# Kernel optimization log

Hardware: AMD Instinct MI355X
Metric: run time of the kernel (lower is better)

## Reference

```python
import jax, jax.numpy as jnp
import numpy as np


def sym_logm(x):
    # matrix log of symmetric positive-definite matrices via eigh
    w, v = jnp.linalg.eigh(x)
    return jnp.einsum('...ik,...k,...jk->...ij', v, jnp.log(w), v)


def olm_diffeo(x):
    s = sym_logm(x)
    L = jnp.tril(s, -1)
    return L + L.swapaxes(-1, -2)


def cayley_map(X):
    I = jnp.eye(X.shape[-1], dtype=X.dtype)
    return (I - X) @ jnp.linalg.inv(I + X)


def trans_base(W, y):
    # C = cayley(skew(W)); y -> sym off-diagonal part of C y C^T
    C = cayley_map(W - W.T)
    y = jnp.einsum('pq,bnqr,sr->bnps', C, y, C)
    L = jnp.tril(y, -1)
    return L + L.swapaxes(-1, -2)


def setup_inputs() -> dict:
    B, N, n = 16, 512, 32
    key = jax.random.key(0)
    k1, k2, k3, k4 = jax.random.split(key, 4)
    A = jax.random.normal(k1, (B, N, n, n), dtype=jnp.float32)
    cov = A @ A.swapaxes(-1, -2) / n + jnp.eye(n, dtype=jnp.float32)
    d = jnp.sqrt(jnp.diagonal(cov, axis1=-2, axis2=-1))
    x = cov / (d[..., :, None] * d[..., None, :])  # SPD correlation matrices
    q_weight = jax.random.normal(k2, (n, n), dtype=jnp.float32) * 2.0 - 1.0
    k_weight = jax.random.normal(k3, (n, n), dtype=jnp.float32) * 2.0 - 1.0
    v_weight = jax.random.normal(k4, (n, n), dtype=jnp.float32) * 2.0 - 1.0
    return {"x": x, "q_weight": q_weight, "k_weight": k_weight, "v_weight": v_weight}


def reference(x, q_weight, k_weight, v_weight):
    xl = olm_diffeo(x)                       # [B,N,n,n]
    q = trans_base(q_weight, xl)
    k = trans_base(k_weight, xl)
    v = trans_base(v_weight, xl)
    B, N, n, _ = q.shape
    qf = q.reshape(B, N, n * n)
    kf = k.reshape(B, N, n * n)
    # energy[b,j,i] = ||q_i - k_j||_F  (Gram trick instead of [B,N,N,n,n] broadcast)
    q2 = jnp.sum(qf * qf, axis=-1)
    k2 = jnp.sum(kf * kf, axis=-1)
    d2 = q2[:, None, :] + k2[:, :, None] - 2.0 * jnp.einsum('bjf,bif->bji', kf, qf)
    energy = jnp.sqrt(jnp.maximum(d2, 1e-12))
    scores = 1.0 / (1.0 + jnp.log1p(energy))
    p = jax.nn.softmax(scores, axis=-2)      # softmax over j (dim -2), as in torch
    attn = p.swapaxes(-1, -2)                # [b, i, j]
    # out[b,c] = sum_a v[b,a] * attn[b,a,c]  (faithful to torch broadcast+sum(dim=1))
    return jnp.einsum('bac,baij->bcij', attn, v)
```

## Files before the change

kernel.cpp:

```cpp
#include <hip/hip_runtime.h>
#include <math.h>

#define NB 16
#define NSQ 512
#define NMAT (NB*NSQ)
#define NF 1024
#define NSWEEP 7
#define SB 36

__global__ __launch_bounds__(64) void cayley_kernel(
    const float* __restrict__ qw, const float* __restrict__ kw,
    const float* __restrict__ vw, float* __restrict__ Cout) {
  __shared__ float M[32][33];
  __shared__ float R[32][33];
  __shared__ float fac[32];
  const float* W = (blockIdx.x == 0) ? qw : ((blockIdx.x == 1) ? kw : vw);
  const int t = threadIdx.x;
  for (int idx = t; idx < 1024; idx += 64) {
    int i = idx >> 5, j = idx & 31;
    float xv = W[i*32+j] - W[j*32+i];
    float d = (i == j) ? 1.0f : 0.0f;
    M[i][j] = d - xv;
    R[i][j] = d + xv;
  }
  __syncthreads();
  for (int k = 0; k < 32; ++k) {
    float inv = 1.0f / M[k][k];
    __syncthreads();
    if (t < 32) M[k][t] *= inv; else R[k][t-32] *= inv;
    __syncthreads();
    if (t < 32) fac[t] = M[t][k];
    __syncthreads();
    if (t < 32) {
      float mk = M[k][t];
      for (int i = 0; i < 32; ++i) {
        if (i == k) continue;
        M[i][t] -= fac[i] * mk;
      }
    } else {
      int tc = t - 32;
      float rk = R[k][tc];
      for (int i = 0; i < 32; ++i) {
        if (i == k) continue;
        R[i][tc] -= fac[i] * rk;
      }
    }
    __syncthreads();
  }
  for (int idx = t; idx < 1024; idx += 64) {
    int p = idx >> 5, q = idx & 31;
    Cout[blockIdx.x * 1024 + idx] = R[q][p];
  }
}

__global__ __launch_bounds__(128) void logm_qkv_kernel(
    const float* __restrict__ x, const float* __restrict__ Cm,
    float* __restrict__ qo, float* __restrict__ ko, float* __restrict__ vo,
    float* __restrict__ q2, float* __restrict__ k2) {
  __shared__ __align__(16) float buf0[32*SB];
  __shared__ __align__(16) float buf1[32*SB];
  __shared__ __align__(16) float buf2[32*SB];
  __shared__ __align__(16) float2 cs[16];
  __shared__ __align__(16) float lw[32];
  __shared__ float wsum[2];
  const int t = threadIdx.x;
  const int m = blockIdx.x;
  const float* xm = x + (size_t)m * NF;

  #pragma unroll
  for (int s = 0; s < 2; ++s) {
    int fi = t + 128*s;
    int i = fi >> 3, j4 = (fi & 7) << 2;
    float4 xv = *(const float4*)&xm[(size_t)fi*4];
    *(float4*)&buf0[i*SB + j4] = xv;
    float4 iv;
    iv.x = (i == j4+0) ? 1.0f : 0.0f;
    iv.y = (i == j4+1) ? 1.0f : 0.0f;
    iv.z = (i == j4+2) ? 1.0f : 0.0f;
    iv.w = (i == j4+3) ? 1.0f : 0.0f;
    *(float4*)&buf1[i*SB + j4] = iv;
  }
  __syncthreads();

  const int abase = t >> 4;
  const int bI = t & 15;
  const int pi = abase & 1;

  for (int sw = 0; sw < NSWEEP; ++sw) {
    for (int r = 1; r < 32; ++r) {
      const int h = 31 - __builtin_clz((unsigned)r);
      const int lowmask = (1 << h) - 1;
      if (t < 16) {
        int p = ((t >> h) << (h+1)) | (t & lowmask);
        int q = p ^ r;
        float apq = buf0[p*SB+q];
        float c = 1.0f, s = 0.0f;
        if (fabsf(apq) > 1e-36f) {
          float app = buf0[p*SB+p];
          float aqq = buf0[q*SB+q];
          float tau = (aqq - app) / (2.0f * apq);
          float tt = 1.0f / (fabsf(tau) + sqrtf(1.0f + tau*tau));
          tt = (tau < 0.0f) ? -tt : tt;
          c = 1.0f / sqrtf(1.0f + tt*tt);
          s = tt * c;
        }
        cs[t] = make_float2(c, s);
      }
      __syncthreads();
      if (r == 1) {
        {
          int pr = t >> 3;
          int ch = (t & 7) << 2;
          int p = pr << 1;
          int q = p | 1;
          float2 c2 = cs[pr];
          float4 ap = *(float4*)&buf0[p*SB + ch];
          float4 aq = *(float4*)&buf0[q*SB + ch];
          float4 np, nq;
          np.x = c2.x*ap.x - c2.y*aq.x;  nq.x = fmaf(c2.y, ap.x, c2.x*aq.x);
          np.y = c2.x*ap.y - c2.y*aq.y;  nq.y = fmaf(c2.y, ap.y, c2.x*aq.y);
          np.z = c2.x*ap.z - c2.y*aq.z;  nq.z = fmaf(c2.y, ap.z, c2.x*aq.z);
          np.w = c2.x*ap.w - c2.y*aq.w;  nq.w = fmaf(c2.y, ap.w, c2.x*aq.w);
          *(float4*)&buf0[p*SB + ch] = np;
          *(float4*)&buf0[q*SB + ch] = nq;
        }
        __syncthreads();
        #pragma unroll
        for (int s4 = 0; s4 < 2; ++s4) {
          int tsk = t + 128*s4;
          int i = tsk >> 3;
          int cch = tsk & 7;
          float2 cA = cs[2*cch];
          float2 cB = cs[2*cch+1];
          float4 y = *(float4*)&buf0[i*SB + 4*cch];
          float4 z;
          z.x = cA.x*y.x - cA.y*y.y;  z.y = fmaf(cA.y, y.x, cA.x*y.y);
          z.z = cB.x*y.z - cB.y*y.w;  z.w = fmaf(cB.y, y.z, cB.x*y.w);
          *(float4*)&buf0[i*SB + 4*cch] = z;
        }
      } else {
        int pb = ((bI >> h) << (h+1)) | (bI & lowmask);
        int qb = pb ^ r;
        if (pi) { int tmp = pb; pb = qb; qb = tmp; }
        const float2 cb2 = cs[bI];
        const float cbb = cb2.x;
        const float sbb = pi ? -cb2.y : cb2.y;
        #pragma unroll
        for (int u = 0; u < 2; ++u) {
          int a = abase + 8*u;
          int pa = ((a >> h) << (h+1)) | (a & lowmask);
          int qa = pa ^ r;
          if (pi) { int tmp = pa; pa = qa; qa = tmp; }
          float2 ca2 = cs[a];
          float caa = ca2.x;
          float saa = pi ? -ca2.y : ca2.y;
          float* rp = buf0 + pa*SB;
          float* rq = buf0 + qa*SB;
          float x11 = rp[pb], x12 = rp[qb];
          float x21 = rq[pb], x22 = rq[qb];
          float y11 = caa*x11 - saa*x21;
          float y12 = caa*x12 - saa*x22;
          float y21 = fmaf(saa, x11, caa*x21);
          float y22 = fmaf(saa, x12, caa*x22);
          rp[pb] = cbb*y11 - sbb*y12;
          rp[qb] = fmaf(sbb, y11, cbb*y12);
          rq[pb] = cbb*y21 - sbb*y22;
          rq[qb] = fmaf(sbb, y21, cbb*y22);
        }
      }
      {
        int pr = t >> 3;
        int ch = (t & 7) << 2;
        int p = ((pr >> h) << (h+1)) | (pr & lowmask);
        int q = p ^ r;
        float2 c2 = cs[pr];
        float4 vp = *(float4*)&buf1[p*SB + ch];
        float4 vq = *(float4*)&buf1[q*SB + ch];
        float4 np, nq;
        np.x = c2.x*vp.x - c2.y*vq.x;  nq.x = fmaf(c2.y, vp.x, c2.x*vq.x);
        np.y = c2.x*vp.y - c2.y*vq.y;  nq.y = fmaf(c2.y, vp.y, c2.x*vq.y);
        np.z = c2.x*vp.z - c2.y*vq.z;  nq.z = fmaf(c2.y, vp.z, c2.x*vq.z);
        np.w = c2.x*vp.w - c2.y*vq.w;  nq.w = fmaf(c2.y, vp.w, c2.x*vq.w);
        *(float4*)&buf1[p*SB + ch] = np;
        *(float4*)&buf1[q*SB + ch] = nq;
      }
      __syncthreads();
    }
  }

  if (t < 32) lw[t] = logf(fmaxf(buf0[t*SB+t], 1e-30f));
  __syncthreads();
  #pragma unroll
  for (int s = 0; s < 8; ++s) {
    int idx = t + 128*s;
    int i = idx >> 5, k = idx & 31;
    buf0[i*SB + k] = buf1[k*SB + i];
  }
  __syncthreads();

  const int rg = t >> 4, cg = t & 15;
  const int i0 = rg*4, j0 = cg*2;
  {
    float acc[4][2] = {};
    #pragma unroll
    for (int k4 = 0; k4 < 32; k4 += 4) {
      float4 lv = *(float4*)&lw[k4];
      float4 av[4], bv[2];
      #pragma unroll
      for (int d = 0; d < 4; ++d) {
        float4 a4 = *(float4*)&buf0[(i0+d)*SB + k4];
        av[d].x = a4.x*lv.x; av[d].y = a4.y*lv.y; av[d].z = a4.z*lv.z; av[d].w = a4.w*lv.w;
      }
      #pragma unroll
      for (int e = 0; e < 2; ++e)
        bv[e] = *(float4*)&buf0[(j0+e)*SB + k4];
      #pragma unroll
      for (int d = 0; d < 4; ++d)
        #pragma unroll
        for (int e = 0; e < 2; ++e) {
          acc[d][e] = fmaf(av[d].x, bv[e].x, acc[d][e]);
          acc[d][e] = fmaf(av[d].y, bv[e].y, acc[d][e]);
          acc[d][e] = fmaf(av[d].z, bv[e].z, acc[d][e]);
          acc[d][e] = fmaf(av[d].w, bv[e].w, acc[d][e]);
        }
    }
    #pragma unroll
    for (int d = 0; d < 4; ++d) {
      #pragma unroll
      for (int e = 0; e < 2; ++e)
        if (i0+d == j0+e) acc[d][e] = 0.0f;
      float2 z; z.x = acc[d][0]; z.y = acc[d][1];
      *(float2*)&buf1[(i0+d)*SB + j0] = z;
    }
  }
  __syncthreads();

  for (int w = 0; w < 3; ++w) {
    const float* Cw = Cm + w*1024;
    #pragma unroll
    for (int s = 0; s < 2; ++s) {
      int fi = t + 128*s;
      int i = fi >> 3, c4 = (fi & 7) << 2;
      *(float4*)&buf0[i*SB + c4] = *(const float4*)&Cw[fi*4];
    }
    __syncthreads();
    {
      float acc[4][2] = {};
      #pragma unroll
      for (int k4 = 0; k4 < 32; k4 += 4) {
        float4 av[4], bv[2];
        #pragma unroll
        for (int d = 0; d < 4; ++d)
          av[d] = *(float4*)&buf0[(i0+d)*SB + k4];
        #pragma unroll
        for (int e = 0; e < 2; ++e)
          bv[e] = *(float4*)&buf1[(j0+e)*SB + k4];
        #pragma unroll
        for (int d = 0; d < 4; ++d)
          #pragma unroll
          for (int e = 0; e < 2; ++e) {
            acc[d][e] = fmaf(av[d].x, bv[e].x, acc[d][e]);
            acc[d][e] = fmaf(av[d].y, bv[e].y, acc[d][e]);
            acc[d][e] = fmaf(av[d].z, bv[e].z, acc[d][e]);
            acc[d][e] = fmaf(av[d].w, bv[e].w, acc[d][e]);
          }
      }
      #pragma unroll
      for (int d = 0; d < 4; ++d) {
        float2 z; z.x = acc[d][0]; z.y = acc[d][1];
        *(float2*)&buf2[(i0+d)*SB + j0] = z;
      }
    }
    __syncthreads();
    {
      float acc[4][2] = {};
      #pragma unroll
      for (int k4 = 0; k4 < 32; k4 += 4) {
        float4 av[4], bv[2];
        #pragma unroll
        for (int d = 0; d < 4; ++d)
          av[d] = *(float4*)&buf2[(i0+d)*SB + k4];
        #pragma unroll
        for (int e = 0; e < 2; ++e)
          bv[e] = *(float4*)&buf0[(j0+e)*SB + k4];
        #pragma unroll
        for (int d = 0; d < 4; ++d)
          #pragma unroll
          for (int e = 0; e < 2; ++e) {
            acc[d][e] = fmaf(av[d].x, bv[e].x, acc[d][e]);
            acc[d][e] = fmaf(av[d].y, bv[e].y, acc[d][e]);
            acc[d][e] = fmaf(av[d].z, bv[e].z, acc[d][e]);
            acc[d][e] = fmaf(av[d].w, bv[e].w, acc[d][e]);
          }
      }
      float ss = 0.0f;
      float* outp = (w == 0) ? qo : ((w == 1) ? ko : vo);
      #pragma unroll
      for (int d = 0; d < 4; ++d) {
        #pragma unroll
        for (int e = 0; e < 2; ++e) {
          if (i0+d == j0+e) acc[d][e] = 0.0f;
          ss = fmaf(acc[d][e], acc[d][e], ss);
        }
        float2 z; z.x = acc[d][0]; z.y = acc[d][1];
        *(float2*)&outp[(size_t)m*NF + (i0+d)*32 + j0] = z;
      }
      if (w < 2) {
        #pragma unroll
        for (int off = 32; off > 0; off >>= 1)
          ss += __shfl_down(ss, off);
        if ((t & 63) == 0) wsum[t >> 6] = ss;
      }
      __syncthreads();
      if (w < 2 && t == 0)
        ((w == 0) ? q2 : k2)[m] = wsum[0] + wsum[1];
    }
  }
}

__global__ __launch_bounds__(256) void scores_kernel(
    const float* __restrict__ qf, const float* __restrict__ kf,
    const float* __restrict__ q2, const float* __restrict__ k2,
    float* __restrict__ P) {
  __shared__ float Ks[64][17];
  __shared__ float Qs[64][17];
  const int b = blockIdx.z;
  const int j0 = blockIdx.y * 64;
  const int i0 = blockIdx.x * 64;
  const int tx = threadIdx.x & 15, ty = threadIdx.x >> 4;
  const int lrow = threadIdx.x >> 2;
  const int lc4 = (threadIdx.x & 3) * 4;
  float acc[4][4] = {};
  const float* kb = kf + (size_t)(b*NSQ + j0) * NF;
  const float* qb = qf + (size_t)(b*NSQ + i0) * NF;
  for (int f0 = 0; f0 < NF; f0 += 16) {
    float4 kv = *(const float4*)(kb + (size_t)lrow*NF + f0 + lc4);
    float4 qv = *(const float4*)(qb + (size_t)lrow*NF + f0 + lc4);
    Ks[lrow][lc4+0] = kv.x; Ks[lrow][lc4+1] = kv.y; Ks[lrow][lc4+2] = kv.z; Ks[lrow][lc4+3] = kv.w;
    Qs[lrow][lc4+0] = qv.x; Qs[lrow][lc4+1] = qv.y; Qs[lrow][lc4+2] = qv.z; Qs[lrow][lc4+3] = qv.w;
    __syncthreads();
    #pragma unroll
    for (int kk = 0; kk < 16; ++kk) {
      float a0 = Ks[ty*4+0][kk], a1 = Ks[ty*4+1][kk], a2 = Ks[ty*4+2][kk], a3 = Ks[ty*4+3][kk];
      float b0 = Qs[tx*4+0][kk], b1 = Qs[tx*4+1][kk], b2 = Qs[tx*4+2][kk], b3 = Qs[tx*4+3][kk];
      acc[0][0]=fmaf(a0,b0,acc[0][0]); acc[0][1]=fmaf(a0,b1,acc[0][1]);
      acc[0][2]=fmaf(a0,b2,acc[0][2]); acc[0][3]=fmaf(a0,b3,acc[0][3]);
      acc[1][0]=fmaf(a1,b0,acc[1][0]); acc[1][1]=fmaf(a1,b1,acc[1][1]);
      acc[1][2]=fmaf(a1,b2,acc[1][2]); acc[1][3]=fmaf(a1,b3,acc[1][3]);
      acc[2][0]=fmaf(a2,b0,acc[2][0]); acc[2][1]=fmaf(a2,b1,acc[2][1]);
      acc[2][2]=fmaf(a2,b2,acc[2][2]); acc[2][3]=fmaf(a2,b3,acc[2][3]);
      acc[3][0]=fmaf(a3,b0,acc[3][0]); acc[3][1]=fmaf(a3,b1,acc[3][1]);
      acc[3][2]=fmaf(a3,b2,acc[3][2]); acc[3][3]=fmaf(a3,b3,acc[3][3]);
    }
    __syncthreads();
  }
  #pragma unroll
  for (int u = 0; u < 4; ++u) {
    int j = j0 + ty*4 + u;
    float kj = k2[b*NSQ + j];
    #pragma unroll
    for (int vv = 0; vv < 4; ++vv) {
      int i = i0 + tx*4 + vv;
      float d2 = kj + q2[b*NSQ + i] - 2.0f * acc[u][vv];
      float e = sqrtf(fmaxf(d2, 1e-12f));
      float sc = 1.0f / (1.0f + log1pf(e));
      P[(size_t)(b*NSQ + j)*NSQ + i] = sc;
    }
  }
}

__global__ __launch_bounds__(512) void softmax_kernel(float* __restrict__ P) {
  __shared__ float red[16][32];
  const int b = blockIdx.x >> 4;
  const int i0 = (blockIdx.x & 15) * 32;
  const int il = threadIdx.x & 31;
  const int jg = threadIdx.x >> 5;
  float* base = P + (size_t)b*NSQ*NSQ + i0 + il;
  float mx = -1e30f;
  for (int j = jg*32; j < jg*32 + 32; ++j)
    mx = fmaxf(mx, base[(size_t)j*NSQ]);
  red[jg][il] = mx;
  __syncthreads();
  float cm = red[0][il];
  #pragma unroll
  for (int g = 1; g < 16; ++g) cm = fmaxf(cm, red[g][il]);
  __syncthreads();
  float ssum = 0.0f;
  for (int j = jg*32; j < jg*32 + 32; ++j)
    ssum += expf(base[(size_t)j*NSQ] - cm);
  red[jg][il] = ssum;
  __syncthreads();
  float tot = red[0][il];
  #pragma unroll
  for (int g = 1; g < 16; ++g) tot += red[g][il];
  float inv = 1.0f / tot;
  for (int j = jg*32; j < jg*32 + 32; ++j) {
    size_t o = (size_t)j*NSQ;
    base[o] = expf(base[o] - cm) * inv;
  }
}

__global__ __launch_bounds__(256) void out_gemm_kernel(
    const float* __restrict__ P, const float* __restrict__ vf,
    float* __restrict__ out) {
  __shared__ float Ps[64][17];
  __shared__ float Vs[16][68];
  const int b = blockIdx.z;
  const int c0 = blockIdx.y * 64;
  const int f0 = blockIdx.x * 64;
  const int tx = threadIdx.x & 15, ty = threadIdx.x >> 4;
  float acc[4][4] = {};
  const float* Pb = P + (size_t)b * NSQ * NSQ;
  const float* Vb = vf + (size_t)b * NSQ * NF;
  for (int a0 = 0; a0 < NSQ; a0 += 16) {
    {
      int row = threadIdx.x >> 2;
      int c4 = (threadIdx.x & 3) * 4;
      float4 pv = *(const float4*)(Pb + (size_t)(c0 + row) * NSQ + a0 + c4);
      Ps[row][c4+0]=pv.x; Ps[row][c4+1]=pv.y; Ps[row][c4+2]=pv.z; Ps[row][c4+3]=pv.w;
    }
    {
      int row = threadIdx.x >> 4;
      int c4 = (threadIdx.x & 15) * 4;
      float4 vv4 = *(const float4*)(Vb + (size_t)(a0 + row) * NF + f0 + c4);
      Vs[row][c4+0]=vv4.x; Vs[row][c4+1]=vv4.y; Vs[row][c4+2]=vv4.z; Vs[row][c4+3]=vv4.w;
    }
    __syncthreads();
    #pragma unroll
    for (int kk = 0; kk < 16; ++kk) {
      float a0r = Ps[ty*4+0][kk], a1r = Ps[ty*4+1][kk], a2r = Ps[ty*4+2][kk], a3r = Ps[ty*4+3][kk];
      float b0 = Vs[kk][tx*4+0], b1 = Vs[kk][tx*4+1], b2 = Vs[kk][tx*4+2], b3 = Vs[kk][tx*4+3];
      acc[0][0]=fmaf(a0r,b0,acc[0][0]); acc[0][1]=fmaf(a0r,b1,acc[0][1]);
      acc[0][2]=fmaf(a0r,b2,acc[0][2]); acc[0][3]=fmaf(a0r,b3,acc[0][3]);
      acc[1][0]=fmaf(a1r,b0,acc[1][0]); acc[1][1]=fmaf(a1r,b1,acc[1][1]);
      acc[1][2]=fmaf(a1r,b2,acc[1][2]); acc[1][3]=fmaf(a1r,b3,acc[1][3]);
      acc[2][0]=fmaf(a2r,b0,acc[2][0]); acc[2][1]=fmaf(a2r,b1,acc[2][1]);
      acc[2][2]=fmaf(a2r,b2,acc[2][2]); acc[2][3]=fmaf(a2r,b3,acc[2][3]);
      acc[3][0]=fmaf(a3r,b0,acc[3][0]); acc[3][1]=fmaf(a3r,b1,acc[3][1]);
      acc[3][2]=fmaf(a3r,b2,acc[3][2]); acc[3][3]=fmaf(a3r,b3,acc[3][3]);
    }
    __syncthreads();
  }
  #pragma unroll
  for (int u = 0; u < 4; ++u) {
    float4 o;
    o.x = acc[u][0]; o.y = acc[u][1]; o.z = acc[u][2]; o.w = acc[u][3];
    *(float4*)(out + (size_t)(b*NSQ + c0 + ty*4 + u) * NF + f0 + tx*4) = o;
  }
}

extern "C" void kernel_launch(void* const* d_in, const int* in_sizes, int n_in,
                              void* d_out, int out_size, void* d_ws, size_t ws_size,
                              hipStream_t stream) {
  const float* x  = (const float*)d_in[0];
  const float* qw = (const float*)d_in[1];
  const float* kw = (const float*)d_in[2];
  const float* vw = (const float*)d_in[3];
  float* ws = (float*)d_ws;
  float* C  = ws;
  float* q  = ws + 3072;
  float* k  = q + (size_t)NMAT * NF;
  float* v  = k + (size_t)NMAT * NF;
  float* q2 = v + (size_t)NMAT * NF;
  float* k2 = q2 + NMAT;
  float* P  = k2 + NMAT;
  float* out = (float*)d_out;

  cayley_kernel<<<dim3(3), dim3(64), 0, stream>>>(qw, kw, vw, C);
  logm_qkv_kernel<<<dim3(NMAT), dim3(128), 0, stream>>>(x, C, q, k, v, q2, k2);
  scores_kernel<<<dim3(8, 8, NB), dim3(256), 0, stream>>>(q, k, q2, k2, P);
  softmax_kernel<<<dim3(NB * 16), dim3(512), 0, stream>>>(P);
  out_gemm_kernel<<<dim3(16, 8, NB), dim3(256), 0, stream>>>(P, v, out);
}
```

Before: 1.423 ms.

## Enlarge GEMM tiles to 128x128 with 8x8 register blocking and transposed smem

Both the scores and output GEMM kernels move from 64x64 tiles with 4x4 per-thread outputs to 128x128 tiles with 8x8 per-thread outputs. Shared memory is stored k-major so inner-loop operands come in as float4 loads, and the trailing sync is moved before the store. This raises arithmetic intensity and cuts shared and global traffic per FMA. The cost is far fewer blocks (256 and 512), which can underfill the GPU, plus higher register pressure.

```diff
diff --git a/kernel.cpp b/kernel.cpp
--- a/kernel.cpp
+++ b/kernel.cpp
@@ -322,49 +322,58 @@
     const float* __restrict__ qf, const float* __restrict__ kf,
     const float* __restrict__ q2, const float* __restrict__ k2,
     float* __restrict__ P) {
-  __shared__ float Ks[64][17];
-  __shared__ float Qs[64][17];
+  __shared__ float Ks[16][132];
+  __shared__ float Qs[16][132];
   const int b = blockIdx.z;
-  const int j0 = blockIdx.y * 64;
-  const int i0 = blockIdx.x * 64;
+  const int j0 = blockIdx.y * 128;
+  const int i0 = blockIdx.x * 128;
   const int tx = threadIdx.x & 15, ty = threadIdx.x >> 4;
-  const int lrow = threadIdx.x >> 2;
-  const int lc4 = (threadIdx.x & 3) * 4;
-  float acc[4][4] = {};
+  const int srow = threadIdx.x >> 1;
+  const int sk8  = (threadIdx.x & 1) * 8;
+  float acc[8][8] = {};
   const float* kb = kf + (size_t)(b*NSQ + j0) * NF;
   const float* qb = qf + (size_t)(b*NSQ + i0) * NF;
   for (int f0 = 0; f0 < NF; f0 += 16) {
-    float4 kv = *(const float4*)(kb + (size_t)lrow*NF + f0 + lc4);
-    float4 qv = *(const float4*)(qb + (size_t)lrow*NF + f0 + lc4);
-    Ks[lrow][lc4+0] = kv.x; Ks[lrow][lc4+1] = kv.y; Ks[lrow][lc4+2] = kv.z; Ks[lrow][lc4+3] = kv.w;
-    Qs[lrow][lc4+0] = qv.x; Qs[lrow][lc4+1] = qv.y; Qs[lrow][lc4+2] = qv.z; Qs[lrow][lc4+3] = qv.w;
+    float4 ka = *(const float4*)(kb + (size_t)srow*NF + f0 + sk8);
+    float4 kb4 = *(const float4*)(kb + (size_t)srow*NF + f0 + sk8 + 4);
+    float4 qa = *(const float4*)(qb + (size_t)srow*NF + f0 + sk8);
+    float4 qb4 = *(const float4*)(qb + (size_t)srow*NF + f0 + sk8 + 4);
+    __syncthreads();
+    Ks[sk8+0][srow] = ka.x;  Ks[sk8+1][srow] = ka.y;
+    Ks[sk8+2][srow] = ka.z;  Ks[sk8+3][srow] = ka.w;
+    Ks[sk8+4][srow] = kb4.x; Ks[sk8+5][srow] = kb4.y;
+    Ks[sk8+6][srow] = kb4.z; Ks[sk8+7][srow] = kb4.w;
+    Qs[sk8+0][srow] = qa.x;  Qs[sk8+1][srow] = qa.y;
+    Qs[sk8+2][srow] = qa.z;  Qs[sk8+3][srow] = qa.w;
+    Qs[sk8+4][srow] = qb4.x; Qs[sk8+5][srow] = qb4.y;
+    Qs[sk8+6][srow] = qb4.z; Qs[sk8+7][srow] = qb4.w;
     __syncthreads();
     #pragma unroll
     for (int kk = 0; kk < 16; ++kk) {
-      float a0 = Ks[ty*4+0][kk], a1 = Ks[ty*4+1][kk], a2 = Ks[ty*4+2][kk], a3 = Ks[ty*4+3][kk];
-      float b0 = Qs[tx*4+0][kk], b1 = Qs[tx*4+1][kk], b2 = Qs[tx*4+2][kk], b3 = Qs[tx*4+3][kk];
-      acc[0][0]=fmaf(a0,b0,acc[0][0]); acc[0][1]=fmaf(a0,b1,acc[0][1]);
-      acc[0][2]=fmaf(a0,b2,acc[0][2]); acc[0][3]=fmaf(a0,b3,acc[0][3]);
-      acc[1][0]=fmaf(a1,b0,acc[1][0]); acc[1][1]=fmaf(a1,b1,acc[1][1]);
-      acc[1][2]=fmaf(a1,b2,acc[1][2]); acc[1][3]=fmaf(a1,b3,acc[1][3]);
-      acc[2][0]=fmaf(a2,b0,acc[2][0]); acc[2][1]=fmaf(a2,b1,acc[2][1]);
-      acc[2][2]=fmaf(a2,b2,acc[2][2]); acc[2][3]=fmaf(a2,b3,acc[2][3]);
-      acc[3][0]=fmaf(a3,b0,acc[3][0]); acc[3][1]=fmaf(a3,b1,acc[3][1]);
-      acc[3][2]=fmaf(a3,b2,acc[3][2]); acc[3][3]=fmaf(a3,b3,acc[3][3]);
-    }
-    __syncthreads();
-  }
-  #pragma unroll
-  for (int u = 0; u < 4; ++u) {
-    int j = j0 + ty*4 + u;
+      float4 a0 = *(float4*)&Ks[kk][ty*8];
+      float4 a1 = *(float4*)&Ks[kk][ty*8 + 4];
+      float4 b0 = *(float4*)&Qs[kk][tx*8];
+      float4 b1 = *(float4*)&Qs[kk][tx*8 + 4];
+      float av[8] = {a0.x,a0.y,a0.z,a0.w,a1.x,a1.y,a1.z,a1.w};
+      float bv[8] = {b0.x,b0.y,b0.z,b0.w,b1.x,b1.y,b1.z,b1.w};
+      #pragma unroll
+      for (int d = 0; d < 8; ++d)
+        #pragma unroll
+        for (int e = 0; e < 8; ++e)
+          acc[d][e] = fmaf(av[d], bv[e], acc[d][e]);
+    }
+  }
+  #pragma unroll
+  for (int u = 0; u < 8; ++u) {
+    int j = j0 + ty*8 + u;
     float kj = k2[b*NSQ + j];
-    #pragma unroll
-    for (int vv = 0; vv < 4; ++vv) {
-      int i = i0 + tx*4 + vv;
+    float* prow = P + (size_t)(b*NSQ + j)*NSQ + i0 + tx*8;
+    #pragma unroll
+    for (int vv = 0; vv < 8; ++vv) {
+      int i = i0 + tx*8 + vv;
       float d2 = kj + q2[b*NSQ + i] - 2.0f * acc[u][vv];
       float e = sqrtf(fmaxf(d2, 1e-12f));
-      float sc = 1.0f / (1.0f + log1pf(e));
-      P[(size_t)(b*NSQ + j)*NSQ + i] = sc;
+      prow[vv] = 1.0f / (1.0f + log1pf(e));
     }
   }
 }
@@ -403,49 +412,54 @@
 __global__ __launch_bounds__(256) void out_gemm_kernel(
     const float* __restrict__ P, const float* __restrict__ vf,
     float* __restrict__ out) {
-  __shared__ float Ps[64][17];
-  __shared__ float Vs[16][68];
+  __shared__ float Ps[16][132];
+  __shared__ float Vs[16][132];
   const int b = blockIdx.z;
-  const int c0 = blockIdx.y * 64;
-  const int f0 = blockIdx.x * 64;
+  const int c0 = blockIdx.y * 128;
+  const int f0 = blockIdx.x * 128;
   const int tx = threadIdx.x & 15, ty = threadIdx.x >> 4;
-  float acc[4][4] = {};
+  const int srow = threadIdx.x >> 1;
+  const int sk8  = (threadIdx.x & 1) * 8;
+  const int vrow = threadIdx.x >> 4;
+  const int vc8  = (threadIdx.x & 15) * 8;
+  float acc[8][8] = {};
   const float* Pb = P + (size_t)b * NSQ * NSQ;
   const float* Vb = vf + (size_t)b * NSQ * NF;
   for (int a0 = 0; a0 < NSQ; a0 += 16) {
-    {
-      int row = threadIdx.x >> 2;
-      int c4 = (threadIdx.x & 3) * 4;
-      float4 pv = *(const float4*)(Pb + (size_t)(c0 + row) * NSQ + a0 + c4);
-      Ps[row][c4+0]=pv.x; Ps[row][c4+1]=pv.y; Ps[row][c4+2]=pv.z; Ps[row][c4+3]=pv.w;
-    }
-    {
-      int row = threadIdx.x >> 4;
-      int c4 = (threadIdx.x & 15) * 4;
-      float4 vv4 = *(const float4*)(Vb + (size_t)(a0 + row) * NF + f0 + c4);
-      Vs[row][c4+0]=vv4.x; Vs[row][c4+1]=vv4.y; Vs[row][c4+2]=vv4.z; Vs[row][c4+3]=vv4.w;
-    }
+    float4 pa = *(const float4*)(Pb + (size_t)(c0 + srow)*NSQ + a0 + sk8);
+    float4 pb4 = *(const float4*)(Pb + (size_t)(c0 + srow)*NSQ + a0 + sk8 + 4);
+    float4 va = *(const float4*)(Vb + (size_t)(a0 + vrow)*NF + f0 + vc8);
+    float4 vb4 = *(const float4*)(Vb + (size_t)(a0 + vrow)*NF + f0 + vc8 + 4);
+    __syncthreads();
+    Ps[sk8+0][srow] = pa.x;  Ps[sk8+1][srow] = pa.y;
+    Ps[sk8+2][srow] = pa.z;  Ps[sk8+3][srow] = pa.w;
+    Ps[sk8+4][srow] = pb4.x; Ps[sk8+5][srow] = pb4.y;
+    Ps[sk8+6][srow] = pb4.z; Ps[sk8+7][srow] = pb4.w;
+    *(float4*)&Vs[vrow][vc8] = va;
+    *(float4*)&Vs[vrow][vc8 + 4] = vb4;
     __syncthreads();
     #pragma unroll
     for (int kk = 0; kk < 16; ++kk) {
-      float a0r = Ps[ty*4+0][kk], a1r = Ps[ty*4+1][kk], a2r = Ps[ty*4+2][kk], a3r = Ps[ty*4+3][kk];
-      float b0 = Vs[kk][tx*4+0], b1 = Vs[kk][tx*4+1], b2 = Vs[kk][tx*4+2], b3 = Vs[kk][tx*4+3];
-      acc[0][0]=fmaf(a0r,b0,acc[0][0]); acc[0][1]=fmaf(a0r,b1,acc[0][1]);
-      acc[0][2]=fmaf(a0r,b2,acc[0][2]); acc[0][3]=fmaf(a0r,b3,acc[0][3]);
-      acc[1][0]=fmaf(a1r,b0,acc[1][0]); acc[1][1]=fmaf(a1r,b1,acc[1][1]);
-      acc[1][2]=fmaf(a1r,b2,acc[1][2]); acc[1][3]=fmaf(a1r,b3,acc[1][3]);
-      acc[2][0]=fmaf(a2r,b0,acc[2][0]); acc[2][1]=fmaf(a2r,b1,acc[2][1]);
-      acc[2][2]=fmaf(a2r,b2,acc[2][2]); acc[2][3]=fmaf(a2r,b3,acc[2][3]);
-      acc[3][0]=fmaf(a3r,b0,acc[3][0]); acc[3][1]=fmaf(a3r,b1,acc[3][1]);
-      acc[3][2]=fmaf(a3r,b2,acc[3][2]); acc[3][3]=fmaf(a3r,b3,acc[3][3]);
-    }
-    __syncthreads();
-  }
-  #pragma unroll
-  for (int u = 0; u < 4; ++u) {
-    float4 o;
-    o.x = acc[u][0]; o.y = acc[u][1]; o.z = acc[u][2]; o.w = acc[u][3];
-    *(float4*)(out + (size_t)(b*NSQ + c0 + ty*4 + u) * NF + f0 + tx*4) = o;
+      float4 a0v = *(float4*)&Ps[kk][ty*8];
+      float4 a1v = *(float4*)&Ps[kk][ty*8 + 4];
+      float4 b0v = *(float4*)&Vs[kk][tx*8];
+      float4 b1v = *(float4*)&Vs[kk][tx*8 + 4];
+      float av[8] = {a0v.x,a0v.y,a0v.z,a0v.w,a1v.x,a1v.y,a1v.z,a1v.w};
+      float bv[8] = {b0v.x,b0v.y,b0v.z,b0v.w,b1v.x,b1v.y,b1v.z,b1v.w};
+      #pragma unroll
+      for (int d = 0; d < 8; ++d)
+        #pragma unroll
+        for (int e = 0; e < 8; ++e)
+          acc[d][e] = fmaf(av[d], bv[e], acc[d][e]);
+    }
+  }
+  #pragma unroll
+  for (int u = 0; u < 8; ++u) {
+    float* orow = out + (size_t)(b*NSQ + c0 + ty*8 + u) * NF + f0 + tx*8;
+    float4 o0; o0.x = acc[u][0]; o0.y = acc[u][1]; o0.z = acc[u][2]; o0.w = acc[u][3];
+    float4 o1; o1.x = acc[u][4]; o1.y = acc[u][5]; o1.z = acc[u][6]; o1.w = acc[u][7];
+    *(float4*)orow = o0;
+    *(float4*)(orow + 4) = o1;
   }
 }
 
@@ -468,7 +482,7 @@
 
   cayley_kernel<<<dim3(3), dim3(64), 0, stream>>>(qw, kw, vw, C);
   logm_qkv_kernel<<<dim3(NMAT), dim3(128), 0, stream>>>(x, C, q, k, v, q2, k2);
-  scores_kernel<<<dim3(8, 8, NB), dim3(256), 0, stream>>>(q, k, q2, k2, P);
+  scores_kernel<<<dim3(4, 4, NB), dim3(256), 0, stream>>>(q, k, q2, k2, P);
   softmax_kernel<<<dim3(NB * 16), dim3(512), 0, stream>>>(P);
-  out_gemm_kernel<<<dim3(16, 8, NB), dim3(256), 0, stream>>>(P, v, out);
-}
+  out_gemm_kernel<<<dim3(8, 4, NB), dim3(256), 0, stream>>>(P, v, out);
+}
```

After: 1.369 ms. 3.8% less time.
